# Optimization experiments

Hardware: AMD Instinct MI355X
Metric: run time of the kernel (lower is better)

Reference implementation:

```python
import jax, jax.numpy as jnp
import numpy as np

B, N, IC, PC, OUT = 2, 4096, 256, 128, 128
BN_EPS = 1e-5


def setup_inputs() -> dict:
    key = jax.random.key(0)
    ks = jax.random.split(key, 6)
    return {
        "point_features": jax.random.normal(ks[0], (B, PC, N), jnp.float32),
        "img_features": jax.random.normal(ks[1], (B, IC, N), jnp.float32),
        "fc2_w": jax.random.normal(ks[2], (PC, IC), jnp.float32) * (1.0 / np.sqrt(IC)),
        "fc2_b": jax.random.normal(ks[3], (PC,), jnp.float32) * 0.01,
        "conv_w": jax.random.normal(ks[4], (OUT, 2 * PC), jnp.float32) * (1.0 / np.sqrt(2 * PC)),
        "conv_b": jax.random.normal(ks[5], (OUT,), jnp.float32) * 0.01,
        "bn_gamma": jnp.ones((OUT,), jnp.float32),
        "bn_beta": jnp.zeros((OUT,), jnp.float32),
        "bn_mean": jnp.zeros((OUT,), jnp.float32),
        "bn_var": jnp.ones((OUT,), jnp.float32),
    }


def reference(point_features, img_features, fc2_w, fc2_b, conv_w, conv_b,
              bn_gamma, bn_beta, bn_mean, bn_var):
    # IA_layer3 (dropout in eval mode -> identity)
    rp = jnp.swapaxes(point_features, 1, 2)            # [B, N, pc]
    ri = jnp.swapaxes(img_features, 1, 2) @ fc2_w.T + fc2_b  # fc2: [B, N, pc]
    scale = 1.0 / np.sqrt(PC).astype(np.float32)

    # scores = rp @ ri^T / sqrt(d); softmax over dim=1 (the rp-token axis)
    s_p = jnp.einsum('bnd,bmd->bnm', rp, ri) * scale   # [B, N, N]
    aw_p = jax.nn.softmax(s_p, axis=1)
    out_p = jnp.einsum('bij,bjd->bid', aw_p, rp)       # [B, N, pc]

    s_i = jnp.einsum('bnd,bmd->bnm', ri, rp) * scale   # [B, N, N]
    aw_i = jax.nn.softmax(s_i, axis=1)
    out_i = jnp.einsum('bij,bjd->bid', aw_i, ri)       # [B, N, pc]

    # fuse: permute to channel-first, concat on channels -> [B, 2*pc, N]
    fusion = jnp.concatenate([jnp.swapaxes(out_p, 1, 2),
                              jnp.swapaxes(out_i, 1, 2)], axis=1)
    # conv1d(k=1) + BN(eval) + ReLU, all per-channel elementwise over N
    y = jnp.einsum('oc,bcn->bon', conv_w, fusion) + conv_b[None, :, None]
    inv_std = jax.lax.rsqrt(bn_var + BN_EPS)
    y = (y - bn_mean[None, :, None]) * (bn_gamma * inv_std)[None, :, None] \
        + bn_beta[None, :, None]
    return jax.nn.relu(y)                              # [B, OUT, N]
```

## Files before the change

### kernel.cpp

```cpp
#include <hip/hip_runtime.h>
#include <math.h>

#define NTOK 4096
#define PCH  128
#define ICH  256
#define OCH  128
#define NB   2
#define SCALEF 0.08838834764831845f
#define SCALE2 0.12751743f

typedef __bf16 bf16_t;
typedef __attribute__((ext_vector_type(8))) __bf16 bf16x8;
typedef __attribute__((ext_vector_type(4))) __bf16 bf16x4;
typedef __attribute__((ext_vector_type(4))) float floatx4;

#define LDK 136

__global__ __launch_bounds__(256) void pack_all(const float* __restrict__ pf,
                                                const float* __restrict__ img,
                                                bf16_t* __restrict__ pfC,
                                                bf16_t* __restrict__ pfT,
                                                bf16_t* __restrict__ imgT)
{
    __shared__ float Ls[64][65];
    const int t = threadIdx.x;
    const int n0 = blockIdx.x * 64, b = blockIdx.z;
    const bool ispf = blockIdx.y < 2;
    const int d0 = ispf ? blockIdx.y * 64 : (blockIdx.y - 2) * 64;
    const float* src = (ispf ? pf + ((size_t)(b * PCH + d0)) * NTOK
                             : img + ((size_t)(b * ICH + d0)) * NTOK) + n0;
#pragma unroll
    for (int p = 0; p < 4; p++) {
        int d = p * 16 + (t >> 4), c = t & 15;
        float4 v = *(const float4*)&src[d * NTOK + c * 4];
        Ls[d][c * 4 + 0] = v.x; Ls[d][c * 4 + 1] = v.y;
        Ls[d][c * 4 + 2] = v.z; Ls[d][c * 4 + 3] = v.w;
        if (ispf) {
            bf16x4 o = { (bf16_t)v.x, (bf16_t)v.y, (bf16_t)v.z, (bf16_t)v.w };
            *(bf16x4*)&pfC[((size_t)(b * PCH + d0 + d)) * NTOK + n0 + c * 4] = o;
        }
    }
    __syncthreads();
#pragma unroll
    for (int p = 0; p < 2; p++) {
        int n = p * 32 + (t >> 3), c = t & 7;
        bf16x8 o;
#pragma unroll
        for (int k = 0; k < 8; k++) o[k] = (bf16_t)Ls[c * 8 + k][n];
        if (ispf)
            *(bf16x8*)&pfT[((size_t)(b * NTOK + n0 + n)) * PCH + d0 + c * 8] = o;
        else
            *(bf16x8*)&imgT[((size_t)(b * NTOK + n0 + n)) * ICH + d0 + c * 8] = o;
    }
}

__global__ __launch_bounds__(256) void fc2_mfma(const bf16_t* __restrict__ imgT,
                                                const float* __restrict__ w,
                                                const float* __restrict__ bias,
                                                bf16_t* __restrict__ riC,
                                                bf16_t* __restrict__ riT,
                                                float* __restrict__ zsums)
{
    const int t = threadIdx.x;
    if (blockIdx.y == 0 && blockIdx.z == 0)
        zsums[blockIdx.x * 256 + t] = 0.f;

    const int n0 = blockIdx.x * 64, pbase = blockIdx.y * 64, b = blockIdx.z;
    const int lane = t & 63, wv = t >> 6, tx = lane & 15, q = lane >> 4;
    const int n = n0 + wv * 16 + tx;
    const bf16_t* trow = imgT + ((size_t)(b * NTOK + n)) * ICH;

    floatx4 acc[4];
#pragma unroll
    for (int ot = 0; ot < 4; ot++) acc[ot] = (floatx4){0.f, 0.f, 0.f, 0.f};

#pragma unroll
    for (int s = 0; s < 8; s++) {
        bf16x8 bf = *(const bf16x8*)&trow[s * 32 + q * 8];
#pragma unroll
        for (int ot = 0; ot < 4; ot++) {
            const float* wr = w + (size_t)(pbase + ot * 16 + tx) * ICH + s * 32 + q * 8;
            float4 x0 = *(const float4*)wr;
            float4 x1 = *(const float4*)(wr + 4);
            bf16x8 af;
            af[0] = (bf16_t)x0.x; af[1] = (bf16_t)x0.y; af[2] = (bf16_t)x0.z; af[3] = (bf16_t)x0.w;
            af[4] = (bf16_t)x1.x; af[5] = (bf16_t)x1.y; af[6] = (bf16_t)x1.z; af[7] = (bf16_t)x1.w;
            acc[ot] = __builtin_amdgcn_mfma_f32_16x16x32_bf16(af, bf, acc[ot], 0, 0, 0);
        }
    }

#pragma unroll
    for (int ot = 0; ot < 4; ot++) {
        bf16x4 tv;
#pragma unroll
        for (int r = 0; r < 4; r++) {
            const int p = pbase + ot * 16 + q * 4 + r;
            float v = acc[ot][r] + bias[p];
            tv[r] = (bf16_t)v;
            riC[((size_t)(b * PCH + p)) * NTOK + n] = (bf16_t)v;
        }
        *(bf16x4*)&riT[((size_t)(b * NTOK + n)) * PCH + pbase + ot * 16 + q * 4] = tv;
    }
}

__global__ __launch_bounds__(256, 4) void stats_mfma(const bf16_t* __restrict__ pfT,
                                                     const bf16_t* __restrict__ riT,
                                                     float* __restrict__ zr,
                                                     float* __restrict__ zc,
                                                     float* __restrict__ fus)
{
    __shared__ bf16_t As[64 * LDK];
    __shared__ float zacc[1024];
    const int t = threadIdx.x;
    const int blk = blockIdx.x;

    {
        float4* f4 = (float4*)fus + ((size_t)blk * 256 + t) * 4;
        f4[0] = float4{0.f, 0.f, 0.f, 0.f};
        f4[1] = float4{0.f, 0.f, 0.f, 0.f};
        f4[2] = float4{0.f, 0.f, 0.f, 0.f};
        f4[3] = float4{0.f, 0.f, 0.f, 0.f};
    }

    const int g = blk & 7, slot = blk >> 3;
    const int b = g & 1, js = g >> 1;
    const bf16_t* At = pfT + (size_t)b * NTOK * PCH;
    const bf16_t* Bt = riT + (size_t)b * NTOK * PCH;
    float* zrow = zr + (size_t)b * NTOK;
    float* zcol = zc + (size_t)b * NTOK;
    const int lane = t & 63, w = t >> 6, tx = lane & 15, q = lane >> 4;
    const int i0 = slot * 64;
    const int jbase = js * 1024;
    const int sr = t >> 4, sc = t & 15;
    const bf16_t* Brow = Bt + (size_t)(jbase + w * 16 + tx) * PCH;

    bf16x8 bcur[4];
#pragma unroll
    for (int s = 0; s < 4; s++)
        bcur[s] = *(const bf16x8*)&Brow[s * 32 + q * 8];
#pragma unroll
    for (int p = 0; p < 4; p++) {
        int i = p * 16 + sr;
        *(uint4*)&As[i * LDK + sc * 8] = *(const uint4*)&At[((size_t)(i0 + i)) * PCH + sc * 8];
    }
    __syncthreads();
    bf16x8 af[4][4];
#pragma unroll
    for (int mt = 0; mt < 4; mt++)
#pragma unroll
        for (int s = 0; s < 4; s++)
            af[mt][s] = *(bf16x8*)&As[(mt * 16 + tx) * LDK + s * 32 + q * 8];

    float racc[4] = {0.f, 0.f, 0.f, 0.f};
    for (int jt = 0; jt < 16; jt++) {
        __builtin_amdgcn_s_barrier();
        floatx4 sacc[4];
#pragma unroll
        for (int mt = 0; mt < 4; mt++) {
            sacc[mt] = (floatx4){0.f, 0.f, 0.f, 0.f};
#pragma unroll
            for (int s = 0; s < 4; s++)
                sacc[mt] = __builtin_amdgcn_mfma_f32_16x16x32_bf16(bcur[s], af[mt][s], sacc[mt], 0, 0, 0);
        }
        if (jt < 15) {
            const bf16_t* bn = Brow + (size_t)(jt + 1) * 64 * PCH;
#pragma unroll
            for (int s = 0; s < 4; s++)
                bcur[s] = *(const bf16x8*)&bn[s * 32 + q * 8];
        }

        float ctmp[4] = {0.f, 0.f, 0.f, 0.f};
#pragma unroll
        for (int mt = 0; mt < 4; mt++)
#pragma unroll
            for (int r = 0; r < 4; r++) {
                float e = __expf(sacc[mt][r] * SCALEF);
                racc[mt] += e;
                ctmp[r]  += e;
            }
#pragma unroll
        for (int r = 0; r < 4; r++) {
            float v = ctmp[r];
            v += __shfl_xor(v, 1); v += __shfl_xor(v, 2);
            v += __shfl_xor(v, 4); v += __shfl_xor(v, 8);
            if (tx == 0) zacc[jt * 64 + w * 16 + q * 4 + r] = v;
        }
    }
#pragma unroll
    for (int mt = 0; mt < 4; mt++) {
        float v = racc[mt];
        v += __shfl_xor(v, 16);
        v += __shfl_xor(v, 32);
        if (q == 0) atomicAdd(&zrow[i0 + mt * 16 + tx], v);
    }
    __syncthreads();
#pragma unroll
    for (int k = 0; k < 4; k++)
        atomicAdd(&zcol[jbase + k * 256 + t], zacc[k * 256 + t]);
}

__global__ __launch_bounds__(256, 2) void attn_mfma(const bf16_t* __restrict__ pfT,
                                                    const bf16_t* __restrict__ riT,
                                                    const bf16_t* __restrict__ pfC,
                                                    const bf16_t* __restrict__ riC,
                                                    const float* __restrict__ zrsum,
                                                    const float* __restrict__ zcsum,
                                                    float* __restrict__ fus)
{
    __shared__ char smem[34816];
    bf16_t* As = (bf16_t*)smem;
    char*   Bs = smem;
    char*   Vs = smem + 17408;
    float*  Rs = (float*)smem;

    const int t = threadIdx.x;
    const int blk = blockIdx.x;
    const int g = blk & 7;
    const int slot = blk >> 3;
    const int b = g & 1, mode = (g >> 1) & 1, js = g >> 2;
    const bf16_t* At = (mode == 0 ? pfT : riT) + (size_t)b * NTOK * PCH;
    const bf16_t* Bt = (mode == 0 ? riT : pfT) + (size_t)b * NTOK * PCH;
    const bf16_t* Vc = (mode == 0 ? pfC : riC) + (size_t)b * PCH * NTOK;
    const float* wsum = (mode == 0 ? zcsum : zrsum) + (size_t)b * NTOK;
    const int lane = t & 63, w = t >> 6, tx = lane & 15, q = lane >> 4;
    const int h = w & 1, jh = w >> 1;
    const int i0 = slot * 64;
    const int jbase = js * 2048;
    const int sr = t >> 4, sc = t & 15;

#pragma unroll
    for (int p = 0; p < 4; p++) {
        int i = p * 16 + sr;
        *(uint4*)&As[i * LDK + sc * 8] = *(const uint4*)&At[((size_t)(i0 + i)) * PCH + sc * 8];
    }
    __syncthreads();
    bf16x8 af[2][4];
#pragma unroll
    for (int mt = 0; mt < 2; mt++)
#pragma unroll
        for (int s = 0; s < 4; s++)
            af[mt][s] = *(bf16x8*)&As[(h * 32 + mt * 16 + tx) * LDK + s * 32 + q * 8];
    __syncthreads();

    const float* Wp = wsum + jbase + jh * 32 + q * 4;

    const char* BsrcB = (const char*)Bt + (size_t)jbase * 256 + t * 16;
    const char* VsrcB = (const char*)Vc + (size_t)(t >> 3) * (NTOK * 2)
                        + (size_t)jbase * 2 + (t & 7) * 16;
    char* Bdst = Bs + (t >> 4) * 272 + (t & 15) * 16;
    char* Vdst = Vs + (t >> 3) * 136 + (t & 7) * 16;

    uint4 sB0, sB1, sB2, sB3, sV0, sV1, sV2, sV3;

#define STAGE_ISSUE(jtn)                                                        \
    sB0 = *(const uint4*)(BsrcB + (size_t)(jtn) * 16384);                       \
    sB1 = *(const uint4*)(BsrcB + (size_t)(jtn) * 16384 + 4096);                \
    sB2 = *(const uint4*)(BsrcB + (size_t)(jtn) * 16384 + 8192);                \
    sB3 = *(const uint4*)(BsrcB + (size_t)(jtn) * 16384 + 12288);               \
    sV0 = *(const uint4*)(VsrcB + (size_t)(jtn) * 128);                         \
    sV1 = *(const uint4*)(VsrcB + (size_t)(jtn) * 128 + (size_t)32 * NTOK * 2); \
    sV2 = *(const uint4*)(VsrcB + (size_t)(jtn) * 128 + (size_t)64 * NTOK * 2); \
    sV3 = *(const uint4*)(VsrcB + (size_t)(jtn) * 128 + (size_t)96 * NTOK * 2);

#define STAGE_WRITE()                  \
    *(uint4*)(Bdst)            = sB0;  \
    *(uint4*)(Bdst + 16 * 272) = sB1;  \
    *(uint4*)(Bdst + 32 * 272) = sB2;  \
    *(uint4*)(Bdst + 48 * 272) = sB3;  \
    *(uint4*)(Vdst)            = sV0;  \
    *(uint4*)(Vdst + 32 * 136) = sV1;  \
    *(uint4*)(Vdst + 64 * 136) = sV2;  \
    *(uint4*)(Vdst + 96 * 136) = sV3;

    STAGE_ISSUE(0)
    STAGE_WRITE()
    float4 wv0 = *(const float4*)&Wp[0];
    float4 wv1 = *(const float4*)&Wp[16];
    float4 wn0 = wv0, wn1 = wv1;
    __syncthreads();

    floatx4 acc[2][8];
#pragma unroll
    for (int mt = 0; mt < 2; mt++)
#pragma unroll
        for (int c = 0; c < 8; c++) acc[mt][c] = (floatx4){0.f, 0.f, 0.f, 0.f};

#pragma unroll 1
    for (int jt = 0; jt < 32; jt++) {
        if (jt < 31) {
            STAGE_ISSUE(jt + 1)
            wn0 = *(const float4*)&Wp[(jt + 1) * 64];
            wn1 = *(const float4*)&Wp[(jt + 1) * 64 + 16];
        }
        __builtin_amdgcn_sched_barrier(0);

        bf16x8 bcur[2][4];
#pragma unroll
        for (int jm = 0; jm < 2; jm++)
#pragma unroll
            for (int s = 0; s < 4; s++)
                bcur[jm][s] = *(const bf16x8*)(Bs + (jh * 32 + jm * 16 + tx) * 272 + s * 64 + q * 16);
        bf16x8 vcur[8];
#pragma unroll
        for (int c = 0; c < 8; c++) {
            const char* vb = Vs + (tx + c * 16) * 136 + (jh * 32 + q * 4) * 2;
            bf16x4 vlo = *(const bf16x4*)vb;
            bf16x4 vhi = *(const bf16x4*)(vb + 32);
            vcur[c] = __builtin_shufflevector(vlo, vhi, 0, 1, 2, 3, 4, 5, 6, 7);
        }

        __builtin_amdgcn_s_setprio(1);
        floatx4 sx[2][2];
#pragma unroll
        for (int jm = 0; jm < 2; jm++)
#pragma unroll
            for (int mt = 0; mt < 2; mt++) {
                sx[jm][mt] = (floatx4){0.f, 0.f, 0.f, 0.f};
#pragma unroll
                for (int s = 0; s < 4; s++)
                    sx[jm][mt] = __builtin_amdgcn_mfma_f32_16x16x32_bf16(bcur[jm][s], af[mt][s], sx[jm][mt], 0, 0, 0);
            }
        __builtin_amdgcn_s_setprio(0);

        float lz00 = __builtin_amdgcn_logf(wv0.x), lz01 = __builtin_amdgcn_logf(wv0.y);
        float lz02 = __builtin_amdgcn_logf(wv0.z), lz03 = __builtin_amdgcn_logf(wv0.w);
        float lz10 = __builtin_amdgcn_logf(wv1.x), lz11 = __builtin_amdgcn_logf(wv1.y);
        float lz12 = __builtin_amdgcn_logf(wv1.z), lz13 = __builtin_amdgcn_logf(wv1.w);
        bf16x8 ea0 = {
            (bf16_t)__builtin_amdgcn_exp2f(sx[0][0][0] * SCALE2 - lz00),
            (bf16_t)__builtin_amdgcn_exp2f(sx[0][0][1] * SCALE2 - lz01),
            (bf16_t)__builtin_amdgcn_exp2f(sx[0][0][2] * SCALE2 - lz02),
            (bf16_t)__builtin_amdgcn_exp2f(sx[0][0][3] * SCALE2 - lz03),
            (bf16_t)__builtin_amdgcn_exp2f(sx[1][0][0] * SCALE2 - lz10),
            (bf16_t)__builtin_amdgcn_exp2f(sx[1][0][1] * SCALE2 - lz11),
            (bf16_t)__builtin_amdgcn_exp2f(sx[1][0][2] * SCALE2 - lz12),
            (bf16_t)__builtin_amdgcn_exp2f(sx[1][0][3] * SCALE2 - lz13) };
        bf16x8 ea1 = {
            (bf16_t)__builtin_amdgcn_exp2f(sx[0][1][0] * SCALE2 - lz00),
            (bf16_t)__builtin_amdgcn_exp2f(sx[0][1][1] * SCALE2 - lz01),
            (bf16_t)__builtin_amdgcn_exp2f(sx[0][1][2] * SCALE2 - lz02),
            (bf16_t)__builtin_amdgcn_exp2f(sx[0][1][3] * SCALE2 - lz03),
            (bf16_t)__builtin_amdgcn_exp2f(sx[1][1][0] * SCALE2 - lz10),
            (bf16_t)__builtin_amdgcn_exp2f(sx[1][1][1] * SCALE2 - lz11),
            (bf16_t)__builtin_amdgcn_exp2f(sx[1][1][2] * SCALE2 - lz12),
            (bf16_t)__builtin_amdgcn_exp2f(sx[1][1][3] * SCALE2 - lz13) };

        __syncthreads();

        if (jt < 31) { STAGE_WRITE() }

        __builtin_amdgcn_s_setprio(1);
#pragma unroll
        for (int c = 0; c < 8; c++) {
            acc[0][c] = __builtin_amdgcn_mfma_f32_16x16x32_bf16(ea0, vcur[c], acc[0][c], 0, 0, 0);
            acc[1][c] = __builtin_amdgcn_mfma_f32_16x16x32_bf16(ea1, vcur[c], acc[1][c], 0, 0, 0);
        }
        __builtin_amdgcn_s_setprio(0);

        __syncthreads();
        wv0 = wn0; wv1 = wn1;
    }
#undef STAGE_ISSUE
#undef STAGE_WRITE

    __syncthreads();
#pragma unroll
    for (int half = 0; half < 2; half++) {
        for (int k = t; k < 64 * 65; k += 256) Rs[k] = 0.f;
        __syncthreads();
#pragma unroll
        for (int mt = 0; mt < 2; mt++)
#pragma unroll
            for (int c = 0; c < 4; c++)
#pragma unroll
                for (int r = 0; r < 4; r++)
                    atomicAdd(&Rs[(h * 32 + mt * 16 + q * 4 + r) * 65 + c * 16 + tx],
                              acc[mt][half * 4 + c][r]);
        __syncthreads();
        {
            float* fo = fus + ((size_t)(b * NTOK + i0)) * 256 + mode * 128 + half * 64;
#pragma unroll
            for (int k = 0; k < 16; k++) {
                const int row = w * 16 + k;
                atomicAdd(&fo[(size_t)row * 256 + lane], Rs[row * 65 + lane]);
            }
        }
        __syncthreads();
    }
}

__global__ __launch_bounds__(256) void conv_mfma(const float* __restrict__ fus,
                                                 const float* __restrict__ cw,
                                                 const float* __restrict__ cb,
                                                 const float* __restrict__ g,
                                                 const float* __restrict__ be,
                                                 const float* __restrict__ mu,
                                                 const float* __restrict__ var,
                                                 float* __restrict__ out)
{
    const int t = threadIdx.x;
    const int n0 = blockIdx.x * 64, obase = blockIdx.y * 64, b = blockIdx.z;
    const int lane = t & 63, wv = t >> 6, tx = lane & 15, q = lane >> 4;
    const int n = n0 + wv * 16 + tx;
    const float* frow = fus + ((size_t)(b * NTOK + n)) * 256;

    floatx4 acc[4];
#pragma unroll
    for (int ot = 0; ot < 4; ot++) acc[ot] = (floatx4){0.f, 0.f, 0.f, 0.f};

#pragma unroll
    for (int s = 0; s < 8; s++) {
        float4 f0 = *(const float4*)&frow[s * 32 + q * 8];
        float4 f1 = *(const float4*)&frow[s * 32 + q * 8 + 4];
        bf16x8 bf;
        bf[0] = (bf16_t)f0.x; bf[1] = (bf16_t)f0.y; bf[2] = (bf16_t)f0.z; bf[3] = (bf16_t)f0.w;
        bf[4] = (bf16_t)f1.x; bf[5] = (bf16_t)f1.y; bf[6] = (bf16_t)f1.z; bf[7] = (bf16_t)f1.w;
#pragma unroll
        for (int ot = 0; ot < 4; ot++) {
            const float* wr = cw + (size_t)(obase + ot * 16 + tx) * 256 + s * 32 + q * 8;
            float4 x0 = *(const float4*)wr;
            float4 x1 = *(const float4*)(wr + 4);
            bf16x8 af;
            af[0] = (bf16_t)x0.x; af[1] = (bf16_t)x0.y; af[2] = (bf16_t)x0.z; af[3] = (bf16_t)x0.w;
            af[4] = (bf16_t)x1.x; af[5] = (bf16_t)x1.y; af[6] = (bf16_t)x1.z; af[7] = (bf16_t)x1.w;
            acc[ot] = __builtin_amdgcn_mfma_f32_16x16x32_bf16(af, bf, acc[ot], 0, 0, 0);
        }
    }

#pragma unroll
    for (int ot = 0; ot < 4; ot++)
#pragma unroll
        for (int r = 0; r < 4; r++) {
            const int o = obase + ot * 16 + q * 4 + r;
            const float sc = g[o] * rsqrtf(var[o] + 1e-5f);
            const float b0 = be[o] + (cb[o] - mu[o]) * sc;
            float y = acc[ot][r] * sc + b0;
            out[((size_t)(b * OCH + o)) * NTOK + n] = fmaxf(y, 0.f);
        }
}

extern "C" void kernel_launch(void* const* d_in, const int* in_sizes, int n_in,
                              void* d_out, int out_size, void* d_ws, size_t ws_size,
                              hipStream_t stream)
{
    const float* pf   = (const float*)d_in[0];
    const float* img  = (const float*)d_in[1];
    const float* fc2w = (const float*)d_in[2];
    const float* fc2b = (const float*)d_in[3];
    const float* cw   = (const float*)d_in[4];
    const float* cb   = (const float*)d_in[5];
    const float* g    = (const float*)d_in[6];
    const float* be   = (const float*)d_in[7];
    const float* mu   = (const float*)d_in[8];
    const float* var  = (const float*)d_in[9];
    float* out = (float*)d_out;

    float* fus   = (float*)d_ws;
    float* zrsum = fus + (size_t)NB * NTOK * 256;
    float* zcsum = zrsum + NB * NTOK;
    bf16_t* pfC = (bf16_t*)(zcsum + NB * NTOK);
    bf16_t* pfT = pfC + (size_t)NB * PCH * NTOK;
    bf16_t* riC = pfT + (size_t)NB * NTOK * PCH;
    bf16_t* riT = riC + (size_t)NB * PCH * NTOK;
    bf16_t* imgT = (bf16_t*)fus;

    pack_all  <<<dim3(64, 6, NB), 256, 0, stream>>>(pf, img, pfC, pfT, imgT);
    fc2_mfma  <<<dim3(64, 2, NB), 256, 0, stream>>>(imgT, fc2w, fc2b, riC, riT, zrsum);
    stats_mfma<<<dim3(512),       256, 0, stream>>>(pfT, riT, zrsum, zcsum, fus);
    attn_mfma <<<dim3(512),       256, 0, stream>>>(pfT, riT, pfC, riC, zrsum, zcsum, fus);
    conv_mfma <<<dim3(64, 2, NB), 256, 0, stream>>>(fus, cw, cb, g, be, mu, var, out);
}
```

Before: 234.9 us.

## Give each wave private swizzled LDS staging buffers and drop block barriers

The shared B/V staging tiles are replaced with per-wave private LDS regions. Each wave now loads its own 32-token slice of keys and values, stored with XOR swizzles to avoid bank conflicts, so the two __syncthreads per loop iteration and the one before the loop can be removed. In exchange, waves that share the same j-slice load duplicate data from global memory, doubling staging traffic per block. LDS use per block rises to 64KB, which may limit occupancy.

Result: slower. 328.4 us (+39.8%).

```diff
diff --git a/kernel.cpp b/kernel.cpp
--- a/kernel.cpp
+++ b/kernel.cpp
@@ -207,10 +207,8 @@
                                                     const float* __restrict__ zcsum,
                                                     float* __restrict__ fus)
 {
-    __shared__ char smem[34816];
+    __shared__ char smem[65536];
     bf16_t* As = (bf16_t*)smem;
-    char*   Bs = smem;
-    char*   Vs = smem + 17408;
     float*  Rs = (float*)smem;
 
     const int t = threadIdx.x;
@@ -242,42 +240,64 @@
             af[mt][s] = *(bf16x8*)&As[(h * 32 + mt * 16 + tx) * LDK + s * 32 + q * 8];
     __syncthreads();
 
+    char* Bw = smem + w * 16384;
+    char* Vw = Bw + 8192;
+
+    const char* BsrcB = (const char*)Bt + (size_t)(jbase + jh * 32) * 256 + lane * 16;
+    const char* VsrcB = (const char*)Vc + (size_t)(lane >> 2) * (NTOK * 2)
+                        + (size_t)(jbase + jh * 32) * 2 + (lane & 3) * 16;
+    const int bu = (lane & 15) ^ (lane >> 4);
+    char* BdstE = Bw + (lane >> 4) * 256 + (bu << 4);
+    char* BdstO = Bw + (lane >> 4) * 256 + ((bu ^ 4) << 4);
+    char* Vdst  = Vw + (lane >> 2) * 64 + (((lane & 3) ^ ((lane >> 4) & 3)) << 4);
+
     const float* Wp = wsum + jbase + jh * 32 + q * 4;
-
-    const char* BsrcB = (const char*)Bt + (size_t)jbase * 256 + t * 16;
-    const char* VsrcB = (const char*)Vc + (size_t)(t >> 3) * (NTOK * 2)
-                        + (size_t)jbase * 2 + (t & 7) * 16;
-    char* Bdst = Bs + (t >> 4) * 272 + (t & 15) * 16;
-    char* Vdst = Vs + (t >> 3) * 136 + (t & 7) * 16;
-
-    uint4 sB0, sB1, sB2, sB3, sV0, sV1, sV2, sV3;
-
-#define STAGE_ISSUE(jtn)                                                        \
-    sB0 = *(const uint4*)(BsrcB + (size_t)(jtn) * 16384);                       \
-    sB1 = *(const uint4*)(BsrcB + (size_t)(jtn) * 16384 + 4096);                \
-    sB2 = *(const uint4*)(BsrcB + (size_t)(jtn) * 16384 + 8192);                \
-    sB3 = *(const uint4*)(BsrcB + (size_t)(jtn) * 16384 + 12288);               \
-    sV0 = *(const uint4*)(VsrcB + (size_t)(jtn) * 128);                         \
-    sV1 = *(const uint4*)(VsrcB + (size_t)(jtn) * 128 + (size_t)32 * NTOK * 2); \
-    sV2 = *(const uint4*)(VsrcB + (size_t)(jtn) * 128 + (size_t)64 * NTOK * 2); \
-    sV3 = *(const uint4*)(VsrcB + (size_t)(jtn) * 128 + (size_t)96 * NTOK * 2);
-
-#define STAGE_WRITE()                  \
-    *(uint4*)(Bdst)            = sB0;  \
-    *(uint4*)(Bdst + 16 * 272) = sB1;  \
-    *(uint4*)(Bdst + 32 * 272) = sB2;  \
-    *(uint4*)(Bdst + 48 * 272) = sB3;  \
-    *(uint4*)(Vdst)            = sV0;  \
-    *(uint4*)(Vdst + 32 * 136) = sV1;  \
-    *(uint4*)(Vdst + 64 * 136) = sV2;  \
-    *(uint4*)(Vdst + 96 * 136) = sV3;
+    const int vroff = tx * 64 + (((q >> 1) ^ ((tx >> 2) & 3)) << 4) + ((q & 1) << 3);
+
+    uint4 sB0, sB1, sB2, sB3, sB4, sB5, sB6, sB7;
+    uint4 sV0, sV1, sV2, sV3, sV4, sV5, sV6, sV7;
+
+#define STAGE_ISSUE(jtn)                                                       \
+    sB0 = *(const uint4*)(BsrcB + (size_t)(jtn) * 16384);                      \
+    sB1 = *(const uint4*)(BsrcB + (size_t)(jtn) * 16384 + 1024);               \
+    sB2 = *(const uint4*)(BsrcB + (size_t)(jtn) * 16384 + 2048);               \
+    sB3 = *(const uint4*)(BsrcB + (size_t)(jtn) * 16384 + 3072);               \
+    sB4 = *(const uint4*)(BsrcB + (size_t)(jtn) * 16384 + 4096);               \
+    sB5 = *(const uint4*)(BsrcB + (size_t)(jtn) * 16384 + 5120);               \
+    sB6 = *(const uint4*)(BsrcB + (size_t)(jtn) * 16384 + 6144);               \
+    sB7 = *(const uint4*)(BsrcB + (size_t)(jtn) * 16384 + 7168);               \
+    sV0 = *(const uint4*)(VsrcB + (size_t)(jtn) * 128);                        \
+    sV1 = *(const uint4*)(VsrcB + (size_t)(jtn) * 128 + (size_t)1 * 131072);   \
+    sV2 = *(const uint4*)(VsrcB + (size_t)(jtn) * 128 + (size_t)2 * 131072);   \
+    sV3 = *(const uint4*)(VsrcB + (size_t)(jtn) * 128 + (size_t)3 * 131072);   \
+    sV4 = *(const uint4*)(VsrcB + (size_t)(jtn) * 128 + (size_t)4 * 131072);   \
+    sV5 = *(const uint4*)(VsrcB + (size_t)(jtn) * 128 + (size_t)5 * 131072);   \
+    sV6 = *(const uint4*)(VsrcB + (size_t)(jtn) * 128 + (size_t)6 * 131072);   \
+    sV7 = *(const uint4*)(VsrcB + (size_t)(jtn) * 128 + (size_t)7 * 131072);
+
+#define STAGE_WRITE()                 \
+    *(uint4*)(BdstE)         = sB0;   \
+    *(uint4*)(BdstO + 1024)  = sB1;   \
+    *(uint4*)(BdstE + 2048)  = sB2;   \
+    *(uint4*)(BdstO + 3072)  = sB3;   \
+    *(uint4*)(BdstE + 4096)  = sB4;   \
+    *(uint4*)(BdstO + 5120)  = sB5;   \
+    *(uint4*)(BdstE + 6144)  = sB6;   \
+    *(uint4*)(BdstO + 7168)  = sB7;   \
+    *(uint4*)(Vdst)          = sV0;   \
+    *(uint4*)(Vdst + 1024)   = sV1;   \
+    *(uint4*)(Vdst + 2048)   = sV2;   \
+    *(uint4*)(Vdst + 3072)   = sV3;   \
+    *(uint4*)(Vdst + 4096)   = sV4;   \
+    *(uint4*)(Vdst + 5120)   = sV5;   \
+    *(uint4*)(Vdst + 6144)   = sV6;   \
+    *(uint4*)(Vdst + 7168)   = sV7;
 
     STAGE_ISSUE(0)
     STAGE_WRITE()
     float4 wv0 = *(const float4*)&Wp[0];
     float4 wv1 = *(const float4*)&Wp[16];
     float4 wn0 = wv0, wn1 = wv1;
-    __syncthreads();
 
     floatx4 acc[2][8];
 #pragma unroll
@@ -299,13 +319,14 @@
         for (int jm = 0; jm < 2; jm++)
 #pragma unroll
             for (int s = 0; s < 4; s++)
-                bcur[jm][s] = *(const bf16x8*)(Bs + (jh * 32 + jm * 16 + tx) * 272 + s * 64 + q * 16);
+                bcur[jm][s] = *(const bf16x8*)(Bw + ((jm * 16 + tx) << 8)
+                                               + ((((s * 4) + q) ^ (tx & 7)) << 4));
         bf16x8 vcur[8];
 #pragma unroll
         for (int c = 0; c < 8; c++) {
-            const char* vb = Vs + (tx + c * 16) * 136 + (jh * 32 + q * 4) * 2;
-            bf16x4 vlo = *(const bf16x4*)vb;
-            bf16x4 vhi = *(const bf16x4*)(vb + 32);
+            const char* vp = Vw + vroff + c * 1024;
+            bf16x4 vlo = *(const bf16x4*)vp;
+            bf16x4 vhi = *(const bf16x4*)((const char*)((size_t)vp ^ 32));
             vcur[c] = __builtin_shufflevector(vlo, vhi, 0, 1, 2, 3, 4, 5, 6, 7);
         }
 
@@ -345,8 +366,6 @@
             (bf16_t)__builtin_amdgcn_exp2f(sx[1][1][2] * SCALE2 - lz12),
             (bf16_t)__builtin_amdgcn_exp2f(sx[1][1][3] * SCALE2 - lz13) };
 
-        __syncthreads();
-
         if (jt < 31) { STAGE_WRITE() }
 
         __builtin_amdgcn_s_setprio(1);
@@ -357,7 +376,6 @@
         }
         __builtin_amdgcn_s_setprio(0);
 
-        __syncthreads();
         wv0 = wn0; wv1 = wn1;
     }
 #undef STAGE_ISSUE
```
